# Performance work log

Measured on AMD Instinct MI355X. Metric: run time of the kernel, lower is better.

## Reference

```python
import jax, jax.numpy as jnp
import numpy as np

S, D = 4096, 512


def setup_inputs() -> dict:
    key = jax.random.key(0)
    ks = jax.random.split(key, 10)
    names = ['x', 'w_ql', 'w_kl', 'w_qr', 'w_kr', 'w_qg', 'w_kg', 'w_qloc', 'w_kloc', 'w_v']
    shapes = [(S, D)] + [(D, D)] * 9
    scale = [1.0] + [float(np.sqrt(2.0 / (D + D)))] * 9  # xavier-ish for weights
    return {n: jax.random.normal(k, sh, dtype=jnp.float32) * s
            for n, k, sh, s in zip(names, ks, shapes, scale)}


def reference(x, w_ql, w_kl, w_qr, w_kr, w_qg, w_kg, w_qloc, w_kloc, w_v):
    # x: [S, D]
    s, d = x.shape
    norm = jnp.sqrt(jnp.asarray(d, x.dtype))
    # strict upper triangle (j > i) is masked for the left boundary,
    # strict lower triangle (i > j) for the right boundary
    mask_up = jnp.triu(jnp.ones((s, s), dtype=bool), k=1)

    ql, kl = x @ w_ql, x @ w_kl
    qr, kr = x @ w_qr, x @ w_kr

    neg_inf = jnp.asarray(-jnp.inf, x.dtype)
    left_scores = jnp.where(mask_up, neg_inf, ql @ kl.T) / norm            # [S,S]
    left_boundary = jax.nn.softmax(left_scores, axis=1)
    right_scores = jnp.where(mask_up.T, neg_inf, qr @ kr.T) / norm
    right_boundary = jax.nn.softmax(right_scores, axis=1)

    # left_boundary @ triu(ones)  == forward cumsum along columns
    # right_boundary @ tril(ones) == reverse cumsum along columns
    left_cdf = jnp.cumsum(left_boundary, axis=1)
    right_cdf = jnp.cumsum(right_boundary[:, ::-1], axis=1)[:, ::-1]
    att_mask = left_cdf * right_cdf                                        # [S,S]

    s_glb = (x @ w_qg) @ (x @ w_kg).T                                      # [S,S]
    s_loc = ((x @ w_qloc) @ (x @ w_kloc).T) * att_mask                     # additive local path
    score = (s_glb + s_loc) / norm

    att_weight = jax.nn.softmax(score, axis=1)
    att_output = att_weight @ (x @ w_v)                                    # [S,D]
    return att_output, att_weight
```

## Files before the change

### kernel.cpp

```cpp
#include <hip/hip_runtime.h>


#define SS 4096
#define DD 512
#define INV_NORM 0.04419417382415922f

typedef _Float16 f16;
typedef f16 f16x8 __attribute__((ext_vector_type(8)));
typedef f16 f16x4 __attribute__((ext_vector_type(4)));
typedef float f32x4 __attribute__((ext_vector_type(4)));
typedef unsigned short ushort;
typedef ushort ushort4v __attribute__((ext_vector_type(4)));

#define GAS __attribute__((address_space(1)))
#define LAS __attribute__((address_space(3)))

__device__ __forceinline__ void ldsdma16(const void* g, void* l) {
  __builtin_amdgcn_global_load_lds((const GAS void*)g, (LAS void*)l, 16, 0, 0);
}

__device__ __forceinline__ ushort f2bf(float f) {
  unsigned u = __float_as_uint(f);
  return (ushort)((u + 0x7FFFu + ((u >> 16) & 1u)) >> 16);
}
__device__ __forceinline__ float bf2f(ushort h) {
  return __uint_as_float((unsigned)h << 16);
}

__device__ __forceinline__ void stage16(const f16* __restrict__ src, int ldk, f16* lds, int k0) {
  const int tid  = threadIdx.x;
  const int lane = tid & 63;
  const int wv   = tid >> 6;
  const int rb   = wv * 8 + (lane >> 3);
  const int cs   = lane & 7;
#pragma unroll
  for (int c = 0; c < 4; ++c) {
    const int r = c * 32 + rb;
    const int q = cs ^ (r & 7);
    ldsdma16(src + (size_t)r * ldk + k0 + q * 8, lds + c * 2048 + wv * 512);
  }
}

__device__ __forceinline__ f16x8 fragld(const f16* lds, int r0, int qb) {
  const int lane = threadIdx.x & 63;
  const int r = r0 + (lane & 15);
  const int q = (qb + (lane >> 4)) ^ (r & 7);
  return *(const f16x8*)(lds + r * 64 + q * 8);
}

__device__ __forceinline__ void mma64(const f16* As, const f16* Bs, f32x4 acc[2][8]) {
  const int wv = threadIdx.x >> 6;
#pragma unroll
  for (int ks = 0; ks < 2; ++ks) {
    const f16x8 a0 = fragld(As, wv * 32,      ks * 4);
    const f16x8 a1 = fragld(As, wv * 32 + 16, ks * 4);
#pragma unroll
    for (int j = 0; j < 8; ++j) {
      const f16x8 b = fragld(Bs, j * 16, ks * 4);
      acc[0][j] = __builtin_amdgcn_mfma_f32_16x16x32_f16(a0, b, acc[0][j], 0, 0, 0);
      acc[1][j] = __builtin_amdgcn_mfma_f32_16x16x32_f16(a1, b, acc[1][j], 0, 0, 0);
    }
  }
}

__global__ void k_cvt_x(const float* __restrict__ x, f16* __restrict__ xh) {
  const size_t i = ((size_t)blockIdx.x * 256 + threadIdx.x) * 4;
  const float4 f = *(const float4*)(x + i);
  f16x4 h = { (f16)f.x, (f16)f.y, (f16)f.z, (f16)f.w };
  *(f16x4*)(xh + i) = h;
}

__global__ void k_trw(const float* w0, const float* w1, const float* w2, const float* w3,
                      const float* w4, const float* w5, const float* w6, const float* w7,
                      const float* w8, f16* __restrict__ wt) {
  const float* srcs[9] = {w0, w1, w2, w3, w4, w5, w6, w7, w8};
  const float* src = srcs[blockIdx.z];
  f16* dst = wt + (size_t)blockIdx.z * DD * DD;
  __shared__ float t[32][33];
  const int n0 = blockIdx.x * 32, k0 = blockIdx.y * 32;
  const int tx = threadIdx.x, ty = threadIdx.y;
#pragma unroll
  for (int i = 0; i < 32; i += 8)
    t[ty + i][tx] = src[(size_t)(k0 + ty + i) * DD + n0 + tx];
  __syncthreads();
#pragma unroll
  for (int i = 0; i < 32; i += 8)
    dst[(size_t)(n0 + ty + i) * DD + k0 + tx] = (f16)t[tx][ty + i];
}

__global__ void k_trv(const f16* __restrict__ v, f16* __restrict__ vt) {
  __shared__ f16 t[32][33];
  const int n0 = blockIdx.x * 32, s0 = blockIdx.y * 32;
  const int tx = threadIdx.x, ty = threadIdx.y;
#pragma unroll
  for (int i = 0; i < 32; i += 8)
    t[ty + i][tx] = v[(size_t)(s0 + ty + i) * DD + n0 + tx];
  __syncthreads();
#pragma unroll
  for (int i = 0; i < 32; i += 8)
    vt[(size_t)(n0 + ty + i) * SS + s0 + tx] = t[tx][ty + i];
}

__global__ __launch_bounds__(256, 3) void k_proj(const f16* __restrict__ xh,
                                                 const f16* __restrict__ wt,
                                                 f16* __restrict__ proj) {
  __shared__ __align__(16) f16 As[8192];
  __shared__ __align__(16) f16 Bs[8192];
  const int z = blockIdx.z;
  const f16* B = wt + (size_t)z * DD * DD;
  f16* C = proj + (size_t)z * SS * DD;
  const int R0 = blockIdx.y * 128, C0 = blockIdx.x * 128;
  f32x4 acc[2][8];
#pragma unroll
  for (int i = 0; i < 2; ++i)
#pragma unroll
    for (int j = 0; j < 8; ++j) acc[i][j] = (f32x4){0.f, 0.f, 0.f, 0.f};
  for (int kb = 0; kb < DD / 64; ++kb) {
    __syncthreads();
    stage16(xh + (size_t)R0 * DD, DD, As, kb * 64);
    stage16(B  + (size_t)C0 * DD, DD, Bs, kb * 64);
    __syncthreads();
    mma64(As, Bs, acc);
  }
  const int lane = threadIdx.x & 63, wv = threadIdx.x >> 6;
  const int mm = lane & 15, quad = lane >> 4;
#pragma unroll
  for (int i = 0; i < 2; ++i)
#pragma unroll
    for (int j = 0; j < 8; ++j)
#pragma unroll
      for (int r = 0; r < 4; ++r)
        C[(size_t)(R0 + wv * 32 + i * 16 + quad * 4 + r) * DD + C0 + j * 16 + mm] =
            (f16)acc[i][j][r];
}

__global__ __launch_bounds__(256, 3) void k_bnd(const f16* __restrict__ proj,
                                                f16* __restrict__ eL,
                                                f16* __restrict__ eR) {
  const int t = blockIdx.x, dir = blockIdx.y;
  int rbk = (int)((sqrtf(8.f * t + 1.f) - 1.f) * 0.5f);
  while ((rbk + 1) * (rbk + 2) / 2 <= t) ++rbk;
  while (rbk * (rbk + 1) / 2 > t) --rbk;
  int jt = t - rbk * (rbk + 1) / 2;
  if (dir) { jt = 31 - jt; rbk = 31 - rbk; }
  __shared__ __align__(16) f16 As[8192];
  __shared__ __align__(16) f16 Bs[8192];
  const f16* q  = proj + (size_t)(dir ? 2 : 0) * SS * DD;
  const f16* kp = proj + (size_t)(dir ? 3 : 1) * SS * DD;
  const int R0 = rbk * 128, C0 = jt * 128;
  f32x4 acc[2][8];
#pragma unroll
  for (int i = 0; i < 2; ++i)
#pragma unroll
    for (int j = 0; j < 8; ++j) acc[i][j] = (f32x4){0.f, 0.f, 0.f, 0.f};
  for (int kb = 0; kb < DD / 64; ++kb) {
    __syncthreads();
    stage16(q  + (size_t)R0 * DD, DD, As, kb * 64);
    stage16(kp + (size_t)C0 * DD, DD, Bs, kb * 64);
    __syncthreads();
    mma64(As, Bs, acc);
  }
  const int lane = threadIdx.x & 63, wv = threadIdx.x >> 6;
  const int mm = lane & 15, quad = lane >> 4;
  const bool diag = (jt == rbk);
  f16* outp = dir ? eR : eL;
#pragma unroll
  for (int i = 0; i < 2; ++i)
#pragma unroll
    for (int r = 0; r < 4; ++r) {
      const int rl = wv * 32 + i * 16 + quad * 4 + r;
#pragma unroll
      for (int j = 0; j < 8; ++j) {
        const int cl = j * 16 + mm;
        const float sc = acc[i][j][r] * INV_NORM;
        const bool bad = diag && (dir ? (cl < rl) : (cl > rl));
        const float e = bad ? 0.f : __expf(sc);
        outp[(size_t)(R0 + rl) * SS + (C0 + cl)] = (f16)e;
      }
    }
}

__global__ __launch_bounds__(1024) void k_cumsum(f16* __restrict__ eL,
                                                 const f16* __restrict__ eR) {
  const int i = blockIdx.x;
  const int tid = threadIdx.x, lane = tid & 63, wv = tid >> 6;
  __shared__ float wsL[16], wsR[16];
  const int j0 = tid * 4;

  float pl[4] = {0.f, 0.f, 0.f, 0.f};
  if (j0 <= i) {
    const f16x4 hl = *(const f16x4*)(eL + (size_t)i * SS + j0);
#pragma unroll
    for (int u = 0; u < 4; ++u) pl[u] = (j0 + u <= i) ? (float)hl[u] : 0.f;
  }
#pragma unroll
  for (int u = 1; u < 4; ++u) pl[u] += pl[u - 1];
  const float Tl = pl[3];
  float sl = Tl;
#pragma unroll
  for (int d = 1; d < 64; d <<= 1) {
    const float o = __shfl_up(sl, (unsigned)d, 64);
    if (lane >= d) sl += o;
  }
  if (lane == 63) wsL[wv] = sl;

  float rr[4] = {0.f, 0.f, 0.f, 0.f}, pr[4];
  if (j0 + 3 >= i) {
    const f16x4 hr = *(const f16x4*)(eR + (size_t)i * SS + j0);
#pragma unroll
    for (int u = 0; u < 4; ++u) rr[u] = (j0 + u >= i) ? (float)hr[u] : 0.f;
  }
  pr[0] = rr[0];
#pragma unroll
  for (int u = 1; u < 4; ++u) pr[u] = pr[u - 1] + rr[u];
  const float Tr = pr[3];
  float sr = Tr;
#pragma unroll
  for (int d = 1; d < 64; d <<= 1) {
    const float o = __shfl_up(sr, (unsigned)d, 64);
    if (lane >= d) sr += o;
  }
  if (lane == 63) wsR[wv] = sr;

  __syncthreads();
  float offL = 0.f, totL = 0.f, offR = 0.f, totR = 0.f;
#pragma unroll
  for (int ww = 0; ww < 16; ++ww) {
    const float a = wsL[ww], b = wsR[ww];
    if (ww < wv) { offL += a; offR += b; }
    totL += a; totR += b;
  }
  const float exL = offL + sl - Tl;
  const float exR = offR + sr - Tr;
  const float invL = 1.f / totL, invR = 1.f / totR;

  f16x4 out;
#pragma unroll
  for (int u = 0; u < 4; ++u) {
    const int j = j0 + u;
    const float cdfL = (exL + pl[u]) * invL;
    const float pre  = exR + pr[u];
    const float cdfR = (totR - pre + rr[u]) * invR;
    const float m = (j < i) ? cdfL : ((j > i) ? cdfR : 1.f);
    out[u] = (f16)m;
  }
  *(f16x4*)(eL + (size_t)i * SS + j0) = out;
}

__global__ __launch_bounds__(256, 2) void k_score(const f16* __restrict__ proj,
                                                  const f16* __restrict__ mask,
                                                  f16* __restrict__ ehalf,
                                                  float* __restrict__ lsc) {
  __shared__ __align__(16) f16 Ag[8192];
  __shared__ __align__(16) f16 Bg[8192];
  __shared__ __align__(16) f16 Al[8192];
  __shared__ __align__(16) f16 Bl[8192];
  const int jt = blockIdx.x, rbk = blockIdx.y;
  const f16* qg = proj + (size_t)4 * SS * DD;
  const f16* kg = proj + (size_t)5 * SS * DD;
  const f16* ql = proj + (size_t)6 * SS * DD;
  const f16* kl = proj + (size_t)7 * SS * DD;
  const int R0 = rbk * 128, C0 = jt * 128;
  f32x4 ag[2][8], al[2][8];
#pragma unroll
  for (int i = 0; i < 2; ++i)
#pragma unroll
    for (int j = 0; j < 8; ++j) {
      ag[i][j] = (f32x4){0.f, 0.f, 0.f, 0.f};
      al[i][j] = (f32x4){0.f, 0.f, 0.f, 0.f};
    }
  for (int kb = 0; kb < DD / 64; ++kb) {
    __syncthreads();
    stage16(qg + (size_t)R0 * DD, DD, Ag, kb * 64);
    stage16(kg + (size_t)C0 * DD, DD, Bg, kb * 64);
    stage16(ql + (size_t)R0 * DD, DD, Al, kb * 64);
    stage16(kl + (size_t)C0 * DD, DD, Bl, kb * 64);
    __syncthreads();
    mma64(Ag, Bg, ag);
    mma64(Al, Bl, al);
  }
  const int lane = threadIdx.x & 63, wv = threadIdx.x >> 6;
  const int mm = lane & 15, quad = lane >> 4;
  float ls[2][4];
#pragma unroll
  for (int i = 0; i < 2; ++i)
#pragma unroll
    for (int r = 0; r < 4; ++r) ls[i][r] = 0.f;
#pragma unroll
  for (int i = 0; i < 2; ++i)
#pragma unroll
    for (int r = 0; r < 4; ++r) {
      const int rg = R0 + wv * 32 + i * 16 + quad * 4 + r;
#pragma unroll
      for (int j = 0; j < 8; ++j) {
        const int cg = C0 + j * 16 + mm;
        const float mk = (float)mask[(size_t)rg * SS + cg];
        const float scv = (ag[i][j][r] + al[i][j][r] * mk) * INV_NORM;
        const float e = __expf(scv);
        ehalf[(size_t)rg * SS + cg] = (f16)e;
        ls[i][r] += e;
      }
    }
#pragma unroll
  for (int d = 1; d < 16; d <<= 1)
#pragma unroll
    for (int i = 0; i < 2; ++i)
#pragma unroll
      for (int r = 0; r < 4; ++r)
        ls[i][r] += __shfl_xor(ls[i][r], d, 64);
  if (mm == 0) {
#pragma unroll
    for (int i = 0; i < 2; ++i)
#pragma unroll
      for (int r = 0; r < 4; ++r)
        atomicAdd(&lsc[R0 + wv * 32 + i * 16 + quad * 4 + r], ls[i][r]);
  }
}

__global__ __launch_bounds__(256, 4) void k_pv(const f16* __restrict__ ehalf,
                                               const f16* __restrict__ vt,
                                               ushort* __restrict__ part) {
  __shared__ __align__(16) f16 As[8192];
  __shared__ __align__(16) f16 Bs[8192];
  const int C0 = blockIdx.x * 128, R0 = blockIdx.y * 128, zk = blockIdx.z;
  f32x4 acc[2][8];
#pragma unroll
  for (int i = 0; i < 2; ++i)
#pragma unroll
    for (int j = 0; j < 8; ++j) acc[i][j] = (f32x4){0.f, 0.f, 0.f, 0.f};
  for (int kb = 0; kb < 16; ++kb) {
    const int k0 = zk * 1024 + kb * 64;
    __syncthreads();
    stage16(ehalf + (size_t)R0 * SS, SS, As, k0);
    stage16(vt    + (size_t)C0 * SS, SS, Bs, k0);
    __syncthreads();
    mma64(As, Bs, acc);
  }
  const int lane = threadIdx.x & 63, wv = threadIdx.x >> 6;
  const int mm = lane & 15, quad = lane >> 4;
  ushort* P = part + (size_t)zk * SS * DD;
#pragma unroll
  for (int i = 0; i < 2; ++i)
#pragma unroll
    for (int j = 0; j < 8; ++j)
#pragma unroll
      for (int r = 0; r < 4; ++r)
        P[(size_t)(R0 + wv * 32 + i * 16 + quad * 4 + r) * DD + C0 + j * 16 + mm] =
            f2bf(acc[i][j][r]);
}

__global__ void k_fin(const f16* __restrict__ ehalf, const ushort* __restrict__ part,
                      const float* __restrict__ lsc, float* __restrict__ outw,
                      float* __restrict__ O) {
  const int bx = blockIdx.x;
  if (bx < 8192) {
    const size_t idx = ((size_t)bx * 256 + threadIdx.x) * 8;
    const int row = (int)(idx >> 12);
    const float inv = 1.f / lsc[row];
    const f16x8 h = *(const f16x8*)(ehalf + idx);
    float4 a = { (float)h[0] * inv, (float)h[1] * inv, (float)h[2] * inv, (float)h[3] * inv };
    float4 b = { (float)h[4] * inv, (float)h[5] * inv, (float)h[6] * inv, (float)h[7] * inv };
    *(float4*)(outw + idx) = a;
    *(float4*)(outw + idx + 4) = b;
  } else {
    const size_t idx = ((size_t)(bx - 8192) * 256 + threadIdx.x) * 4;
    const int row = (int)(idx >> 9);
    float s0 = 0.f, s1 = 0.f, s2 = 0.f, s3 = 0.f;
#pragma unroll
    for (int p = 0; p < 4; ++p) {
      const ushort4v v = *(const ushort4v*)(part + (size_t)p * SS * DD + idx);
      s0 += bf2f(v[0]); s1 += bf2f(v[1]); s2 += bf2f(v[2]); s3 += bf2f(v[3]);
    }
    const float inv = 1.f / lsc[row];
    float4 s = { s0 * inv, s1 * inv, s2 * inv, s3 * inv };
    *(float4*)(O + idx) = s;
  }
}

extern "C" void kernel_launch(void* const* d_in, const int* in_sizes, int n_in,
                              void* d_out, int out_size, void* d_ws, size_t ws_size,
                              hipStream_t stream) {
  (void)in_sizes; (void)n_in; (void)out_size; (void)ws_size;
  const float* x = (const float*)d_in[0];
  const float* w[9];
  for (int i = 0; i < 9; ++i) w[i] = (const float*)d_in[1 + i];
  float* O    = (float*)d_out;
  float* outw = O + (size_t)SS * DD;

  char* ws = (char*)d_ws;
  size_t off = 0;
  auto alloc = [&](size_t b) { void* p = ws + off; off += (b + 255) & ~(size_t)255; return p; };
  f16* xh     = (f16*)alloc((size_t)SS * DD * 2);
  f16* wt     = (f16*)alloc((size_t)9 * DD * DD * 2);
  f16* proj   = (f16*)alloc((size_t)9 * SS * DD * 2);
  f16* vt     = (f16*)alloc((size_t)DD * SS * 2);
  f16* eL     = (f16*)alloc((size_t)SS * SS * 2);
  f16* eR     = (f16*)alloc((size_t)SS * SS * 2);
  f16* ehalf  = (f16*)alloc((size_t)SS * SS * 2);
  float* lsc  = (float*)alloc((size_t)SS * 4);
  ushort* part = (ushort*)eR;

  hipMemsetAsync(lsc, 0, (size_t)SS * 4, stream);
  k_cvt_x<<<SS * DD / 1024, 256, 0, stream>>>(x, xh);
  k_trw<<<dim3(16, 16, 9), dim3(32, 8), 0, stream>>>(w[0], w[1], w[2], w[3], w[4],
                                                     w[5], w[6], w[7], w[8], wt);
  k_proj<<<dim3(4, 32, 9), 256, 0, stream>>>(xh, wt, proj);
  k_trv<<<dim3(16, 128), dim3(32, 8), 0, stream>>>(proj + (size_t)8 * SS * DD, vt);
  k_bnd<<<dim3(528, 2), 256, 0, stream>>>(proj, eL, eR);
  k_cumsum<<<SS, 1024, 0, stream>>>(eL, eR);
  k_score<<<dim3(32, 32), 256, 0, stream>>>(proj, eL, ehalf, lsc);
  k_pv<<<dim3(4, 32, 4), 256, 0, stream>>>(ehalf, vt, part);
  k_fin<<<10240, 256, 0, stream>>>(ehalf, part, lsc, outw, O);
}
```

Baseline: 301.0 us.

## Software-pipeline k_score staging and prefetch mask tile into LDS via DMA

Restructures the k_score main loop so the next k-slice of the global and local Q/K tiles is loaded by LDS DMA while the other pair's MFMA runs, with explicit vmcnt waits and raw barriers replacing __syncthreads. It also stages the 128x128 mask tile into the freed global-path LDS buffers during the final local MMA, so the epilogue reads the mask from swizzled LDS instead of issuing scattered global loads. The intent is to hide global load latency and to make the mask reads coalesced. The risk is that the hand-counted vmcnt values and barrier placement are wrong, which would introduce races, and that the extra barriers add stalls.

```diff
diff --git a/kernel.cpp b/kernel.cpp
--- a/kernel.cpp
+++ b/kernel.cpp
@@ -14,6 +14,9 @@
 
 #define GAS __attribute__((address_space(1)))
 #define LAS __attribute__((address_space(3)))
+
+#define BARM() asm volatile("s_barrier" ::: "memory")
+#define WAITV(N) asm volatile("s_waitcnt vmcnt(" #N ")" ::: "memory")
 
 __device__ __forceinline__ void ldsdma16(const void* g, void* l) {
   __builtin_amdgcn_global_load_lds((const GAS void*)g, (LAS void*)l, 16, 0, 0);
@@ -247,6 +250,13 @@
   *(f16x4*)(eL + (size_t)i * SS + j0) = out;
 }
 
+__device__ __forceinline__ float mask_ld(const f16* Am, const f16* Bm, int r, int c) {
+  const f16* b = (c < 64) ? Am : Bm;
+  const int cc = c & 63;
+  const int q = (cc >> 3) ^ (r & 7);
+  return (float)b[r * 64 + q * 8 + (cc & 7)];
+}
+
 __global__ __launch_bounds__(256, 2) void k_score(const f16* __restrict__ proj,
                                                   const f16* __restrict__ mask,
                                                   f16* __restrict__ ehalf,
@@ -269,16 +279,36 @@
       ag[i][j] = (f32x4){0.f, 0.f, 0.f, 0.f};
       al[i][j] = (f32x4){0.f, 0.f, 0.f, 0.f};
     }
-  for (int kb = 0; kb < DD / 64; ++kb) {
-    __syncthreads();
-    stage16(qg + (size_t)R0 * DD, DD, Ag, kb * 64);
-    stage16(kg + (size_t)C0 * DD, DD, Bg, kb * 64);
-    stage16(ql + (size_t)R0 * DD, DD, Al, kb * 64);
-    stage16(kl + (size_t)C0 * DD, DD, Bl, kb * 64);
-    __syncthreads();
+  stage16(qg + (size_t)R0 * DD, DD, Ag, 0);
+  stage16(kg + (size_t)C0 * DD, DD, Bg, 0);
+  stage16(ql + (size_t)R0 * DD, DD, Al, 0);
+  stage16(kl + (size_t)C0 * DD, DD, Bl, 0);
+  for (int kb = 0; kb < DD / 64 - 1; ++kb) {
+    WAITV(8);
+    BARM();
     mma64(Ag, Bg, ag);
+    BARM();
+    stage16(qg + (size_t)R0 * DD, DD, Ag, kb * 64 + 64);
+    stage16(kg + (size_t)C0 * DD, DD, Bg, kb * 64 + 64);
+    WAITV(8);
+    BARM();
     mma64(Al, Bl, al);
-  }
+    BARM();
+    stage16(ql + (size_t)R0 * DD, DD, Al, kb * 64 + 64);
+    stage16(kl + (size_t)C0 * DD, DD, Bl, kb * 64 + 64);
+  }
+  WAITV(8);
+  BARM();
+  mma64(Ag, Bg, ag);
+  BARM();
+  stage16(mask + (size_t)R0 * SS, SS, Ag, C0);
+  stage16(mask + (size_t)R0 * SS, SS, Bg, C0 + 64);
+  WAITV(16);
+  BARM();
+  mma64(Al, Bl, al);
+  WAITV(0);
+  BARM();
+
   const int lane = threadIdx.x & 63, wv = threadIdx.x >> 6;
   const int mm = lane & 15, quad = lane >> 4;
   float ls[2][4];
@@ -290,14 +320,15 @@
   for (int i = 0; i < 2; ++i)
 #pragma unroll
     for (int r = 0; r < 4; ++r) {
-      const int rg = R0 + wv * 32 + i * 16 + quad * 4 + r;
+      const int rl = wv * 32 + i * 16 + quad * 4 + r;
+      const int rg = R0 + rl;
 #pragma unroll
       for (int j = 0; j < 8; ++j) {
-        const int cg = C0 + j * 16 + mm;
-        const float mk = (float)mask[(size_t)rg * SS + cg];
+        const int cl = j * 16 + mm;
+        const float mk = mask_ld(Ag, Bg, rl, cl);
         const float scv = (ag[i][j][r] + al[i][j][r] * mk) * INV_NORM;
         const float e = __expf(scv);
-        ehalf[(size_t)rg * SS + cg] = (f16)e;
+        ehalf[(size_t)rg * SS + (C0 + cl)] = (f16)e;
         ls[i][r] += e;
       }
     }
```

New measurement: 290.6 us. 3.4% less time.

## Load score-kernel MFMA operands directly from global and stage exp output via LDS

Applied to the files above, without the earlier changes.

Drops the LDS-staged tiling loop in k_score. MFMA operands for the two Q·K products now come straight from global memory into registers, with no shared-memory staging and no block barriers. The exp scores are written to a padded per-wave LDS buffer and then stored to ehalf as 16-byte row-contiguous vectors, replacing scattered 2-byte stores. The trade-off is more global (L2) traffic, because each wave re-reads all 128 K rows, and the loads lose the reuse LDS gave them.

```diff
diff --git a/kernel.cpp b/kernel.cpp
--- a/kernel.cpp
+++ b/kernel.cpp
@@ -251,16 +251,16 @@
                                                   const f16* __restrict__ mask,
                                                   f16* __restrict__ ehalf,
                                                   float* __restrict__ lsc) {
-  __shared__ __align__(16) f16 Ag[8192];
-  __shared__ __align__(16) f16 Bg[8192];
-  __shared__ __align__(16) f16 Al[8192];
-  __shared__ __align__(16) f16 Bl[8192];
+  __shared__ __align__(16) f16 rep[4][32][132];
   const int jt = blockIdx.x, rbk = blockIdx.y;
   const f16* qg = proj + (size_t)4 * SS * DD;
   const f16* kg = proj + (size_t)5 * SS * DD;
   const f16* ql = proj + (size_t)6 * SS * DD;
   const f16* kl = proj + (size_t)7 * SS * DD;
   const int R0 = rbk * 128, C0 = jt * 128;
+  const int lane = threadIdx.x & 63, wv = threadIdx.x >> 6;
+  const int mm = lane & 15, quad = lane >> 4;
+
   f32x4 ag[2][8], al[2][8];
 #pragma unroll
   for (int i = 0; i < 2; ++i)
@@ -269,18 +269,30 @@
       ag[i][j] = (f32x4){0.f, 0.f, 0.f, 0.f};
       al[i][j] = (f32x4){0.f, 0.f, 0.f, 0.f};
     }
-  for (int kb = 0; kb < DD / 64; ++kb) {
-    __syncthreads();
-    stage16(qg + (size_t)R0 * DD, DD, Ag, kb * 64);
-    stage16(kg + (size_t)C0 * DD, DD, Bg, kb * 64);
-    stage16(ql + (size_t)R0 * DD, DD, Al, kb * 64);
-    stage16(kl + (size_t)C0 * DD, DD, Bl, kb * 64);
-    __syncthreads();
-    mma64(Ag, Bg, ag);
-    mma64(Al, Bl, al);
-  }
-  const int lane = threadIdx.x & 63, wv = threadIdx.x >> 6;
-  const int mm = lane & 15, quad = lane >> 4;
+
+  const f16* qg0 = qg + (size_t)(R0 + wv * 32 + mm) * DD + quad * 8;
+  const f16* ql0 = ql + (size_t)(R0 + wv * 32 + mm) * DD + quad * 8;
+  const f16* kg0 = kg + (size_t)(C0 + mm) * DD + quad * 8;
+  const f16* kl0 = kl + (size_t)(C0 + mm) * DD + quad * 8;
+
+#pragma unroll 2
+  for (int s = 0; s < 16; ++s) {
+    const int ko = s * 32;
+    const f16x8 aG0 = *(const f16x8*)(qg0 + ko);
+    const f16x8 aG1 = *(const f16x8*)(qg0 + 16 * DD + ko);
+    const f16x8 aL0 = *(const f16x8*)(ql0 + ko);
+    const f16x8 aL1 = *(const f16x8*)(ql0 + 16 * DD + ko);
+#pragma unroll
+    for (int j = 0; j < 8; ++j) {
+      const f16x8 bG = *(const f16x8*)(kg0 + (size_t)(j * 16) * DD + ko);
+      const f16x8 bL = *(const f16x8*)(kl0 + (size_t)(j * 16) * DD + ko);
+      ag[0][j] = __builtin_amdgcn_mfma_f32_16x16x32_f16(aG0, bG, ag[0][j], 0, 0, 0);
+      ag[1][j] = __builtin_amdgcn_mfma_f32_16x16x32_f16(aG1, bG, ag[1][j], 0, 0, 0);
+      al[0][j] = __builtin_amdgcn_mfma_f32_16x16x32_f16(aL0, bL, al[0][j], 0, 0, 0);
+      al[1][j] = __builtin_amdgcn_mfma_f32_16x16x32_f16(aL1, bL, al[1][j], 0, 0, 0);
+    }
+  }
+
   float ls[2][4];
 #pragma unroll
   for (int i = 0; i < 2; ++i)
@@ -290,14 +302,15 @@
   for (int i = 0; i < 2; ++i)
 #pragma unroll
     for (int r = 0; r < 4; ++r) {
-      const int rg = R0 + wv * 32 + i * 16 + quad * 4 + r;
+      const int rl = i * 16 + quad * 4 + r;
+      const int rg = R0 + wv * 32 + rl;
 #pragma unroll
       for (int j = 0; j < 8; ++j) {
-        const int cg = C0 + j * 16 + mm;
-        const float mk = (float)mask[(size_t)rg * SS + cg];
+        const int cl = j * 16 + mm;
+        const float mk = (float)mask[(size_t)rg * SS + (C0 + cl)];
         const float scv = (ag[i][j][r] + al[i][j][r] * mk) * INV_NORM;
         const float e = __expf(scv);
-        ehalf[(size_t)rg * SS + cg] = (f16)e;
+        rep[wv][rl][cl] = (f16)e;
         ls[i][r] += e;
       }
     }
@@ -314,6 +327,17 @@
 #pragma unroll
       for (int r = 0; r < 4; ++r)
         atomicAdd(&lsc[R0 + wv * 32 + i * 16 + quad * 4 + r], ls[i][r]);
+  }
+
+#pragma unroll
+  for (int t = 0; t < 8; ++t) {
+    const int row = t * 4 + quad;
+    const f16x4 v0 = *(const f16x4*)&rep[wv][row][mm * 8];
+    const f16x4 v1 = *(const f16x4*)&rep[wv][row][mm * 8 + 4];
+    f16x8 w;
+    w[0] = v0[0]; w[1] = v0[1]; w[2] = v0[2]; w[3] = v0[3];
+    w[4] = v1[0]; w[5] = v1[1]; w[6] = v1[2]; w[7] = v1[3];
+    *(f16x8*)(ehalf + (size_t)(R0 + wv * 32 + row) * SS + C0 + mm * 8) = w;
   }
 }
 
```

After: 396.5 us. 1.32x slower.
